# Performance work log

Measured on AMD Instinct MI355X. Metric: run time of the kernel, lower is better.

The kernel has to match this reference:

```python
import jax, jax.numpy as jnp
import numpy as np

N, E, D, H, EF = 50000, 800000, 64, 64, 16


def setup_inputs() -> dict:
    key = jax.random.key(0)
    ks = jax.random.split(key, 12)
    s = 0.05
    return {
        "node_feat": jax.random.normal(ks[0], (N, D), jnp.float32),
        "coord": jax.random.normal(ks[1], (N, 3), jnp.float32),
        "edge_feat": jax.random.normal(ks[2], (E, EF), jnp.float32),
        "src": jax.random.randint(ks[3], (E,), 0, N, jnp.int32),
        "dst": jax.random.randint(ks[4], (E,), 0, N, jnp.int32),
        "W_e1": jax.random.normal(ks[5], (2 * D + EF + 1, H), jnp.float32) * s,
        "b_e1": jnp.zeros((H,), jnp.float32),
        "W_e2": jax.random.normal(ks[6], (H, H), jnp.float32) * s,
        "b_e2": jnp.zeros((H,), jnp.float32),
        "W_n1": jax.random.normal(ks[7], (D + H, H), jnp.float32) * s,
        "b_n1": jnp.zeros((H,), jnp.float32),
        "W_n2": jax.random.normal(ks[8], (H, D), jnp.float32) * s,
        "b_n2": jnp.zeros((D,), jnp.float32),
    }


def reference(node_feat, coord, edge_feat, src, dst,
              W_e1, b_e1, W_e2, b_e2, W_n1, b_n1, W_n2, b_n2):
    # per-edge radial distance: ||coord_src - coord_dst||^2  -> [E,1]
    x_diff = coord[src] - coord[dst]
    radial = jnp.sum(x_diff * x_diff, axis=-1, keepdims=True)
    # edge message MLP: concat [h_src, h_dst, radial, a] -> SiLU MLP
    f = jnp.concatenate([node_feat[src], node_feat[dst], radial, edge_feat], axis=-1)
    m = jax.nn.silu(f @ W_e1 + b_e1)
    msg = jax.nn.silu(m @ W_e2 + b_e2)  # [E,H]
    # scatter-sum aggregation to destination nodes
    h_neigh = jax.ops.segment_sum(msg, dst, num_segments=node_feat.shape[0])
    # node update MLP
    z = jnp.concatenate([node_feat, h_neigh], axis=-1)
    h = jax.nn.silu(z @ W_n1 + b_n1) @ W_n2 + b_n2
    return h
```

## Files before the change

kernel.cpp:

```cpp
#include <hip/hip_runtime.h>

#define D 64
#define H 64
#define EFD 16
#define MS 68
#define TE 128
#define TN 128
#define DPB 16
#define DPB4 32
#define REFW 20

typedef __attribute__((ext_vector_type(8))) short bf16x8;
typedef __attribute__((ext_vector_type(4))) float f32x4;

__device__ __forceinline__ float silu(float x) {
    return x / (1.0f + __expf(-x));
}

__device__ __forceinline__ short f2bf(float x) {
    union { float f; unsigned u; } c; c.f = x;
    unsigned r = c.u + 0x7fffu + ((c.u >> 16) & 1u);
    return (short)(r >> 16);
}

#define GEMM_STEP(acc_, a_, bf_) do { \
    const float* bp_ = (const float*)(bf_); \
    acc_[0] += (a_).x*bp_[0] + (a_).y*bp_[4] + (a_).z*bp_[8]  + (a_).w*bp_[12]; \
    acc_[1] += (a_).x*bp_[1] + (a_).y*bp_[5] + (a_).z*bp_[9]  + (a_).w*bp_[13]; \
    acc_[2] += (a_).x*bp_[2] + (a_).y*bp_[6] + (a_).z*bp_[10] + (a_).w*bp_[14]; \
    acc_[3] += (a_).x*bp_[3] + (a_).y*bp_[7] + (a_).z*bp_[11] + (a_).w*bp_[15]; \
} while (0)

#define PGEMM64(acc_, Wp_, wrow0_, eg_, hg_, smem_) do { \
    for (int k4 = 0; k4 < 16; k4++) { \
        float4 bf_[4]; \
        _Pragma("unroll") \
        for (int kk = 0; kk < 4; kk++) \
            bf_[kk] = *(const float4*)&(Wp_)[(size_t)((wrow0_) + 4*k4 + kk) * H + 4*(hg_)]; \
        _Pragma("unroll") \
        for (int i = 0; i < 8; i++) { \
            float4 a_ = *(const float4*)&(smem_)[(8*(eg_) + i) * MS + 4*k4]; \
            GEMM_STEP(acc_[i], a_, bf_); \
        } \
    } \
} while (0)


__global__ __launch_bounds__(256) void hist_kernel(
    const int* __restrict__ dst, int* __restrict__ deg, int E)
{
    int e = blockIdx.x * 256 + threadIdx.x;
    if (e < E) atomicAdd(&deg[dst[e]], 1);
}


__global__ __launch_bounds__(256) void scanA_kernel(
    const int* __restrict__ deg, int* __restrict__ part, int N)
{
    __shared__ int tmp[256];
    const int tid = threadIdx.x;
    int idx = blockIdx.x * 256 + tid;
    tmp[tid] = (idx < N) ? deg[idx] : 0;
    __syncthreads();
    for (int off = 128; off > 0; off >>= 1) {
        if (tid < off) tmp[tid] += tmp[tid + off];
        __syncthreads();
    }
    if (tid == 0) part[blockIdx.x] = tmp[0];
}

__global__ __launch_bounds__(256, 1) void scanB_kernel(
    int* __restrict__ part, int nparts)
{
    __shared__ int tmp[256];
    __shared__ int carry_s;
    const int tid = threadIdx.x;
    if (tid == 0) carry_s = 0;
    __syncthreads();
    for (int base = 0; base < nparts; base += 256) {
        int idx = base + tid;
        int v = (idx < nparts) ? part[idx] : 0;
        tmp[tid] = v;
        __syncthreads();
        #pragma unroll
        for (int off = 1; off < 256; off <<= 1) {
            int t = (tid >= off) ? tmp[tid - off] : 0;
            __syncthreads();
            tmp[tid] += t;
            __syncthreads();
        }
        int incl = tmp[tid];
        int tot = tmp[255];
        if (idx < nparts) part[idx] = carry_s + incl - v;
        __syncthreads();
        if (tid == 0) carry_s += tot;
        __syncthreads();
    }
}

__global__ __launch_bounds__(256) void scanC_kernel(
    const int* __restrict__ deg, const int* __restrict__ part,
    int* __restrict__ cursor, int N)
{
    __shared__ int tmp[256];
    const int tid = threadIdx.x;
    int idx = blockIdx.x * 256 + tid;
    int v = (idx < N) ? deg[idx] : 0;
    tmp[tid] = v;
    __syncthreads();
    #pragma unroll
    for (int off = 1; off < 256; off <<= 1) {
        int t = (tid >= off) ? tmp[tid - off] : 0;
        __syncthreads();
        tmp[tid] += t;
        __syncthreads();
    }
    if (idx < N) cursor[idx] = part[blockIdx.x] + tmp[tid] - v;
}


__global__ __launch_bounds__(256) void build3_kernel(
    const int* __restrict__ dst, const int* __restrict__ src,
    const float* __restrict__ coord, const float* __restrict__ edge_feat,
    int* __restrict__ cursor,
    int* __restrict__ srcs, int* __restrict__ dsts, float* __restrict__ refr,
    int E)
{
    int e = blockIdx.x * 256 + threadIdx.x;
    if (e >= E) return;
    int d2 = dst[e];
    int s = src[e];
    int pos = atomicAdd(&cursor[d2], 1);
    srcs[pos] = s;
    dsts[pos] = d2;
    float dx = coord[s*3+0] - coord[d2*3+0];
    float dy = coord[s*3+1] - coord[d2*3+1];
    float dz = coord[s*3+2] - coord[d2*3+2];
    float* rr = &refr[(size_t)pos * REFW];
    const float4* ef = (const float4*)&edge_feat[(size_t)e * EFD];
    *(float4*)&rr[0]  = ef[0];
    *(float4*)&rr[4]  = ef[1];
    *(float4*)&rr[8]  = ef[2];
    *(float4*)&rr[12] = ef[3];
    rr[16] = dx*dx + dy*dy + dz*dz;
}

__global__ __launch_bounds__(256) void build2_kernel(
    const int* __restrict__ dst, const int* __restrict__ src,
    int* __restrict__ cursor,
    int* __restrict__ eidx, int* __restrict__ srcs, int* __restrict__ dsts,
    int E)
{
    int e = blockIdx.x * 256 + threadIdx.x;
    if (e < E) {
        int d2 = dst[e];
        int pos = atomicAdd(&cursor[d2], 1);
        eidx[pos] = e;
        srcs[pos] = src[e];
        dsts[pos] = d2;
    }
}


__global__ __launch_bounds__(256, 4) void pre_kernel(
    const float* __restrict__ node_feat,
    const float* __restrict__ W_e1, const float* __restrict__ b_e1,
    float* __restrict__ Pa, float* __restrict__ Pb, int N)
{
    __shared__ float smem[TN * MS];
    const int tid = threadIdx.x;
    const int nbase = blockIdx.x * TN;
    const int ng = tid >> 4, hg = tid & 15, k = tid & 63, no = tid >> 6;

    #pragma unroll
    for (int t = 0; t < 32; t++) {
        int gn = nbase + no + 4*t;
        int cg = (gn < N) ? gn : (N - 1);
        smem[(no + 4*t) * MS + k] = node_feat[(size_t)cg * D + k];
    }
    __syncthreads();

    float accA[8][4], accB[8][4];
    {
        float4 b0 = *(const float4*)&b_e1[4*hg];
        #pragma unroll
        for (int i = 0; i < 8; i++) {
            accA[i][0]=b0.x; accA[i][1]=b0.y; accA[i][2]=b0.z; accA[i][3]=b0.w;
            accB[i][0]=0.f;  accB[i][1]=0.f;  accB[i][2]=0.f;  accB[i][3]=0.f;
        }
    }
    PGEMM64(accA, W_e1, 0,  ng, hg, smem);
    PGEMM64(accB, W_e1, 64, ng, hg, smem);

    #pragma unroll
    for (int i = 0; i < 8; i++) {
        int gn = nbase + 8*ng + i;
        if (gn < N) {
            float4 a; a.x=accA[i][0]; a.y=accA[i][1]; a.z=accA[i][2]; a.w=accA[i][3];
            float4 b; b.x=accB[i][0]; b.y=accB[i][1]; b.z=accB[i][2]; b.w=accB[i][3];
            *(float4*)&Pa[(size_t)gn * H + 4*hg] = a;
            *(float4*)&Pb[(size_t)gn * H + 4*hg] = b;
        }
    }
}


__global__ __launch_bounds__(256, 3) void edge_kernel4(
    const float* __restrict__ Pa, const float* __restrict__ Pb,
    const int* __restrict__ srcs, const int* __restrict__ dsts,
    const float* __restrict__ refr,
    const int* __restrict__ cursor_end, const int* __restrict__ deg,
    const float* __restrict__ W_e1,
    const float* __restrict__ W_e2, const float* __restrict__ b_e2,
    float* __restrict__ h_neigh, int N)
{
    __shared__ alignas(16) short mt[TE * H];
    __shared__ float hacc[DPB4 * H];

    const int tid = threadIdx.x;
    const int lane = tid & 63;
    const int wv = tid >> 6;
    const int lg = lane >> 4;
    const int lc = lane & 15;
    const int eg = tid >> 4;
    const int hg = tid & 15;

    const int dst0 = blockIdx.x * DPB4;
    const int dlast = min(dst0 + DPB4, N) - 1;
    const int rs = cursor_end[dst0] - deg[dst0];
    const int re = cursor_end[dlast];

    for (int i = tid; i < DPB4 * H; i += 256) hacc[i] = 0.f;

    bf16x8 bfr[2][4];
    #pragma unroll
    for (int ks = 0; ks < 2; ks++)
        #pragma unroll
        for (int nf = 0; nf < 4; nf++) {
            bf16x8 v;
            #pragma unroll
            for (int t = 0; t < 8; t++)
                v[t] = f2bf(W_e2[(size_t)(lg*8 + t + 32*ks) * H + 16*nf + lc]);
            bfr[ks][nf] = v;
        }
    float bias[4];
    #pragma unroll
    for (int nf = 0; nf < 4; nf++) bias[nf] = b_e2[16*nf + lc];

    __syncthreads();

    for (int base = rs; base < re; base += TE) {
        float a1[8][4];
        #pragma unroll
        for (int i = 0; i < 8; i++) {
            int p = base + 8*eg + i;
            int pp = (p < re) ? p : (re - 1);
            int s = srcs[pp], d2 = dsts[pp];
            float4 pa = *(const float4*)&Pa[(size_t)s * H + 4*hg];
            float4 pb = *(const float4*)&Pb[(size_t)d2 * H + 4*hg];
            a1[i][0] = pa.x + pb.x; a1[i][1] = pa.y + pb.y;
            a1[i][2] = pa.z + pb.z; a1[i][3] = pa.w + pb.w;
        }
        for (int k4 = 0; k4 < 4; k4++) {
            float4 bf[4];
            #pragma unroll
            for (int kk = 0; kk < 4; kk++)
                bf[kk] = *(const float4*)&W_e1[(size_t)(129 + 4*k4 + kk) * H + 4*hg];
            #pragma unroll
            for (int i = 0; i < 8; i++) {
                int p = base + 8*eg + i;
                int pp = (p < re) ? p : (re - 1);
                float4 a = *(const float4*)&refr[(size_t)pp * REFW + 4*k4];
                GEMM_STEP(a1[i], a, bf);
            }
        }
        {
            float4 b = *(const float4*)&W_e1[(size_t)128 * H + 4*hg];
            #pragma unroll
            for (int i = 0; i < 8; i++) {
                int p = base + 8*eg + i;
                int pp = (p < re) ? p : (re - 1);
                float a = refr[(size_t)pp * REFW + 16];
                a1[i][0] += a*b.x; a1[i][1] += a*b.y;
                a1[i][2] += a*b.z; a1[i][3] += a*b.w;
            }
        }

        #pragma unroll
        for (int i = 0; i < 8; i++) {
            short4 mv;
            mv.x = f2bf(silu(a1[i][0])); mv.y = f2bf(silu(a1[i][1]));
            mv.z = f2bf(silu(a1[i][2])); mv.w = f2bf(silu(a1[i][3]));
            int row = 8*eg + i;
            int sidx = (row * H + 4*hg) ^ (i << 3);
            *(short4*)&mt[sidx] = mv;
        }
        asm volatile("s_waitcnt lgkmcnt(0)" ::: "memory");

        bf16x8 afr[2][2];
        #pragma unroll
        for (int mf = 0; mf < 2; mf++)
            #pragma unroll
            for (int ks = 0; ks < 2; ks++) {
                int row = 32*wv + 16*mf + lc;
                int sidx = (row * H + lg*8 + 32*ks) ^ ((lc & 7) << 3);
                afr[mf][ks] = *(const bf16x8*)&mt[sidx];
            }
        f32x4 c2[2][4];
        #pragma unroll
        for (int mf = 0; mf < 2; mf++)
            #pragma unroll
            for (int nf = 0; nf < 4; nf++) {
                f32x4 cinit = {bias[nf], bias[nf], bias[nf], bias[nf]};
                c2[mf][nf] = cinit;
            }
        #pragma unroll
        for (int ks = 0; ks < 2; ks++)
            #pragma unroll
            for (int mf = 0; mf < 2; mf++)
                #pragma unroll
                for (int nf = 0; nf < 4; nf++)
                    c2[mf][nf] = __builtin_amdgcn_mfma_f32_16x16x32_bf16(
                        afr[mf][ks], bfr[ks][nf], c2[mf][nf], 0, 0, 0);

        #pragma unroll
        for (int mf = 0; mf < 2; mf++) {
            int rb = 32*wv + 16*mf + 4*lg;
            int cur = -1;
            float s0 = 0.f, s1 = 0.f, s2 = 0.f, s3 = 0.f;
            #pragma unroll
            for (int reg = 0; reg < 4; reg++) {
                int p = base + rb + reg;
                if (p < re) {
                    int dl = dsts[p] - dst0;
                    float v0 = silu(c2[mf][0][reg]);
                    float v1 = silu(c2[mf][1][reg]);
                    float v2 = silu(c2[mf][2][reg]);
                    float v3 = silu(c2[mf][3][reg]);
                    if (dl != cur) {
                        if (cur >= 0) {
                            atomicAdd(&hacc[cur*H + lc],      s0);
                            atomicAdd(&hacc[cur*H + 16 + lc], s1);
                            atomicAdd(&hacc[cur*H + 32 + lc], s2);
                            atomicAdd(&hacc[cur*H + 48 + lc], s3);
                        }
                        cur = dl; s0 = v0; s1 = v1; s2 = v2; s3 = v3;
                    } else { s0 += v0; s1 += v1; s2 += v2; s3 += v3; }
                }
            }
            if (cur >= 0) {
                atomicAdd(&hacc[cur*H + lc],      s0);
                atomicAdd(&hacc[cur*H + 16 + lc], s1);
                atomicAdd(&hacc[cur*H + 32 + lc], s2);
                atomicAdd(&hacc[cur*H + 48 + lc], s3);
            }
        }
    }

    __syncthreads();
    #pragma unroll
    for (int t = 0; t < 2; t++) {
        int idx = tid + t*256;
        int dloc = idx >> 4;
        int ch = (idx & 15) * 4;
        int gd = dst0 + dloc;
        if (gd < N)
            *(float4*)&h_neigh[(size_t)gd * H + ch] =
                *(const float4*)&hacc[dloc * H + ch];
    }
}


__global__ __launch_bounds__(256, 4) void edge_kernel2(
    const float* __restrict__ Pa, const float* __restrict__ Pb,
    const float* __restrict__ coord,
    const float* __restrict__ edge_feat,
    const int* __restrict__ eidx, const int* __restrict__ srcs,
    const int* __restrict__ dsts,
    const int* __restrict__ cursor_end, const int* __restrict__ deg,
    const float* __restrict__ W_e1,
    const float* __restrict__ W_e2, const float* __restrict__ b_e2,
    float* __restrict__ h_neigh, int N)
{
    __shared__ float smem[TE * MS];
    __shared__ float hacc[DPB * H];
    __shared__ int ssrc[TE], sdlo[TE], seid[TE];

    const int tid = threadIdx.x;
    const int dst0 = blockIdx.x * DPB;
    const int dlast = min(dst0 + DPB, N) - 1;
    const int rs = cursor_end[dst0] - deg[dst0];
    const int re = cursor_end[dlast];

    for (int i = tid; i < DPB * H; i += 256) hacc[i] = 0.f;

    const int eg = tid >> 4, hg = tid & 15;

    for (int base = rs; base < re; base += TE) {
        const int cnt = min(re - base, TE);
        __syncthreads();

        if (tid < TE) {
            int e = 0, s = 0, dlv = -1;
            float radial = 0.f;
            if (tid < cnt) {
                int p = base + tid;
                e = eidx[p]; s = srcs[p];
                int d2 = dsts[p]; dlv = d2 - dst0;
                float dx = coord[s*3+0] - coord[d2*3+0];
                float dy = coord[s*3+1] - coord[d2*3+1];
                float dz = coord[s*3+2] - coord[d2*3+2];
                radial = dx*dx + dy*dy + dz*dz;
            }
            ssrc[tid] = s; sdlo[tid] = dlv; seid[tid] = e;
            smem[tid * MS + 0] = radial;
        }
        __syncthreads();

        {
            const int k2 = tid & 15, e2 = tid >> 4;
            #pragma unroll
            for (int t = 0; t < 8; t++) {
                int r = e2 + 16*t;
                float v = (sdlo[r] >= 0) ? edge_feat[(size_t)seid[r] * EFD + k2] : 0.f;
                smem[r * MS + 1 + k2] = v;
            }
        }

        float acc[8][4];
        #pragma unroll
        for (int i = 0; i < 8; i++) {
            int r = 8*eg + i;
            int s = ssrc[r];
            int dlv = sdlo[r];
            int drow = (dlv >= 0) ? (dst0 + dlv) : 0;
            float4 pa = *(const float4*)&Pa[(size_t)s * H + 4*hg];
            float4 pb = *(const float4*)&Pb[(size_t)drow * H + 4*hg];
            acc[i][0] = pa.x + pb.x; acc[i][1] = pa.y + pb.y;
            acc[i][2] = pa.z + pb.z; acc[i][3] = pa.w + pb.w;
        }
        __syncthreads();

        for (int k4 = 0; k4 < 4; k4++) {
            float4 bf[4];
            #pragma unroll
            for (int kk = 0; kk < 4; kk++)
                bf[kk] = *(const float4*)&W_e1[(size_t)(128 + 4*k4 + kk) * H + 4*hg];
            #pragma unroll
            for (int i = 0; i < 8; i++) {
                float4 a = *(const float4*)&smem[(8*eg + i) * MS + 4*k4];
                GEMM_STEP(acc[i], a, bf);
            }
        }
        {
            float4 b = *(const float4*)&W_e1[(size_t)144 * H + 4*hg];
            #pragma unroll
            for (int i = 0; i < 8; i++) {
                float a = smem[(8*eg+i)*MS + 16];
                acc[i][0] += a*b.x; acc[i][1] += a*b.y; acc[i][2] += a*b.z; acc[i][3] += a*b.w;
            }
        }
        __syncthreads();

        #pragma unroll
        for (int i = 0; i < 8; i++) {
            float4 mv;
            mv.x = silu(acc[i][0]); mv.y = silu(acc[i][1]);
            mv.z = silu(acc[i][2]); mv.w = silu(acc[i][3]);
            *(float4*)&smem[(8*eg+i)*MS + 4*hg] = mv;
        }
        __syncthreads();

        float acc2[8][4];
        {
            float4 b0 = *(const float4*)&b_e2[4*hg];
            #pragma unroll
            for (int i = 0; i < 8; i++) {
                acc2[i][0]=b0.x; acc2[i][1]=b0.y; acc2[i][2]=b0.z; acc2[i][3]=b0.w;
            }
        }
        PGEMM64(acc2, W_e2, 0, eg, hg, smem);

        float rx=0.f, ry=0.f, rz=0.f, rw=0.f;
        int cur = -1;
        #pragma unroll
        for (int i = 0; i < 8; i++) {
            int r = 8*eg + i;
            int dlv = sdlo[r];
            if (dlv < 0) continue;
            float vx = silu(acc2[i][0]), vy = silu(acc2[i][1]);
            float vz = silu(acc2[i][2]), vw = silu(acc2[i][3]);
            if (dlv != cur) {
                if (cur >= 0) {
                    float* hp = &hacc[cur * H + 4*hg];
                    atomicAdd(&hp[0], rx); atomicAdd(&hp[1], ry);
                    atomicAdd(&hp[2], rz); atomicAdd(&hp[3], rw);
                }
                cur = dlv; rx = vx; ry = vy; rz = vz; rw = vw;
            } else {
                rx += vx; ry += vy; rz += vz; rw += vw;
            }
        }
        if (cur >= 0) {
            float* hp = &hacc[cur * H + 4*hg];
            atomicAdd(&hp[0], rx); atomicAdd(&hp[1], ry);
            atomicAdd(&hp[2], rz); atomicAdd(&hp[3], rw);
        }
    }

    __syncthreads();
    {
        const int dloc = tid >> 4, ch = 4 * (tid & 15);
        int gd = dst0 + dloc;
        if (gd < N) {
            float4 v = *(const float4*)&hacc[dloc * H + ch];
            *(float4*)&h_neigh[(size_t)gd * H + ch] = v;
        }
    }
}


__global__ __launch_bounds__(256, 4) void node_kernel(
    const float* __restrict__ node_feat,
    const float* __restrict__ h_neigh,
    const float* __restrict__ W_n1, const float* __restrict__ b_n1,
    const float* __restrict__ W_n2, const float* __restrict__ b_n2,
    float* __restrict__ out, int N)
{
    __shared__ float smem[TN * MS];

    const int tid = threadIdx.x;
    const int nbase = blockIdx.x * TN;

    const int ng = tid >> 4, hg = tid & 15, k = tid & 63, no = tid >> 6;

    float acc[8][4];
    {
        float4 b0 = *(const float4*)&b_n1[4*hg];
        #pragma unroll
        for (int i = 0; i < 8; i++) {
            acc[i][0]=b0.x; acc[i][1]=b0.y; acc[i][2]=b0.z; acc[i][3]=b0.w;
        }
    }

    float rA[32];
    #pragma unroll
    for (int t = 0; t < 32; t++) {
        int gn = nbase + no + 4*t;
        int cg = (gn < N) ? gn : (N - 1);
        rA[t] = node_feat[(size_t)cg * D + k];
    }
    #pragma unroll
    for (int t = 0; t < 32; t++)
        smem[(no + 4*t) * MS + k] = rA[t];
    __syncthreads();

    float rB[32];
    #pragma unroll
    for (int t = 0; t < 32; t++) {
        int gn = nbase + no + 4*t;
        int cg = (gn < N) ? gn : (N - 1);
        rB[t] = h_neigh[(size_t)cg * H + k];
    }
    PGEMM64(acc, W_n1, 0, ng, hg, smem);
    __syncthreads();

    #pragma unroll
    for (int t = 0; t < 32; t++)
        smem[(no + 4*t) * MS + k] = rB[t];
    __syncthreads();

    PGEMM64(acc, W_n1, 64, ng, hg, smem);
    __syncthreads();

    #pragma unroll
    for (int i = 0; i < 8; i++) {
        float4 mv;
        mv.x = silu(acc[i][0]); mv.y = silu(acc[i][1]);
        mv.z = silu(acc[i][2]); mv.w = silu(acc[i][3]);
        *(float4*)&smem[(8*ng+i)*MS + 4*hg] = mv;
    }
    __syncthreads();

    float acc2[8][4];
    {
        float4 b0 = *(const float4*)&b_n2[4*hg];
        #pragma unroll
        for (int i = 0; i < 8; i++) {
            acc2[i][0]=b0.x; acc2[i][1]=b0.y; acc2[i][2]=b0.z; acc2[i][3]=b0.w;
        }
    }
    PGEMM64(acc2, W_n2, 0, ng, hg, smem);

    #pragma unroll
    for (int i = 0; i < 8; i++) {
        int gn = nbase + 8*ng + i;
        if (gn < N) {
            float4 ov;
            ov.x = acc2[i][0]; ov.y = acc2[i][1]; ov.z = acc2[i][2]; ov.w = acc2[i][3];
            *(float4*)&out[(size_t)gn * D + 4*hg] = ov;
        }
    }
}

extern "C" void kernel_launch(void* const* d_in, const int* in_sizes, int n_in,
                              void* d_out, int out_size, void* d_ws, size_t ws_size,
                              hipStream_t stream)
{
    const float* node_feat = (const float*)d_in[0];
    const float* coord     = (const float*)d_in[1];
    const float* edge_feat = (const float*)d_in[2];
    const int*   src       = (const int*)d_in[3];
    const int*   dst       = (const int*)d_in[4];
    const float* W_e1 = (const float*)d_in[5];
    const float* b_e1 = (const float*)d_in[6];
    const float* W_e2 = (const float*)d_in[7];
    const float* b_e2 = (const float*)d_in[8];
    const float* W_n1 = (const float*)d_in[9];
    const float* b_n1 = (const float*)d_in[10];
    const float* W_n2 = (const float*)d_in[11];
    const float* b_n2 = (const float*)d_in[12];

    const int N = in_sizes[0] / D;
    const int E = in_sizes[3];
    const int NP = (N + 255) / 256;

    const size_t hn_b  = (size_t)N * H * sizeof(float);
    const size_t n_i   = (size_t)N * sizeof(int);
    const size_t e_i   = (size_t)E * sizeof(int);
    const size_t pt_b  = 1024 * sizeof(int);
    const size_t p_b   = (size_t)N * H * sizeof(float);
    const size_t rf_b  = (size_t)E * REFW * sizeof(float);

    const size_t need3 = hn_b + 2*n_i + pt_b + 2*e_i + rf_b + 2*p_b;

    float* h_neigh = (float*)d_ws;

    if (ws_size >= need3) {
        char* p = (char*)d_ws + hn_b;
        int* deg    = (int*)p;   p += n_i;
        int* cursor = (int*)p;   p += n_i;
        int* part   = (int*)p;   p += pt_b;
        int* srcs   = (int*)p;   p += e_i;
        int* dsts   = (int*)p;   p += e_i;
        float* refr = (float*)p; p += rf_b;
        float* Pa   = (float*)p; p += p_b;
        float* Pb   = (float*)p;

        hipMemsetAsync(deg, 0, n_i, stream);
        hist_kernel<<<(E + 255) / 256, 256, 0, stream>>>(dst, deg, E);
        scanA_kernel<<<NP, 256, 0, stream>>>(deg, part, N);
        scanB_kernel<<<1, 256, 0, stream>>>(part, NP);
        scanC_kernel<<<NP, 256, 0, stream>>>(deg, part, cursor, N);
        build3_kernel<<<(E + 255) / 256, 256, 0, stream>>>(dst, src, coord, edge_feat,
                                                           cursor, srcs, dsts, refr, E);
        pre_kernel<<<(N + TN - 1) / TN, 256, 0, stream>>>(node_feat, W_e1, b_e1,
                                                          Pa, Pb, N);
        const int dblocks = (N + DPB4 - 1) / DPB4;
        edge_kernel4<<<dblocks, 256, 0, stream>>>(Pa, Pb, srcs, dsts, refr,
                                                  cursor, deg,
                                                  W_e1, W_e2, b_e2, h_neigh, N);
    } else {
        char* p = (char*)d_ws + hn_b;
        int* deg    = (int*)p;   p += n_i;
        int* cursor = (int*)p;   p += n_i;
        int* part   = (int*)p;   p += pt_b;
        int* eidx   = (int*)p;   p += e_i;
        int* srcs   = (int*)p;   p += e_i;
        int* dsts   = (int*)p;   p += e_i;
        float* Pa   = (float*)p; p += p_b;
        float* Pb   = (float*)p;

        hipMemsetAsync(deg, 0, n_i, stream);
        hist_kernel<<<(E + 255) / 256, 256, 0, stream>>>(dst, deg, E);
        scanA_kernel<<<NP, 256, 0, stream>>>(deg, part, N);
        scanB_kernel<<<1, 256, 0, stream>>>(part, NP);
        scanC_kernel<<<NP, 256, 0, stream>>>(deg, part, cursor, N);
        build2_kernel<<<(E + 255) / 256, 256, 0, stream>>>(dst, src, cursor,
                                                           eidx, srcs, dsts, E);
        pre_kernel<<<(N + TN - 1) / TN, 256, 0, stream>>>(node_feat, W_e1, b_e1,
                                                          Pa, Pb, N);
        const int dblocks2 = (N + DPB - 1) / DPB;
        edge_kernel2<<<dblocks2, 256, 0, stream>>>(Pa, Pb, coord, edge_feat,
                                                   eidx, srcs, dsts, cursor, deg,
                                                   W_e1, W_e2, b_e2, h_neigh, N);
    }

    const int nblocks = (N + TN - 1) / TN;
    node_kernel<<<nblocks, 256, 0, stream>>>(node_feat, h_neigh,
                                             W_n1, b_n1, W_n2, b_n2,
                                             (float*)d_out, N);
}
```

Baseline: 525.8 us.

## Fuse node MLP into edge kernel and drop precomputed edge-record buffer

Removes the build3 pass that wrote a per-edge record (edge features plus radial) in sorted order. The edge kernel now gathers edge_feat through eidx and computes the radial from coord on the fly. The node update MLP is appended to the edge kernel using bf16 MFMA on the block's aggregated h_neigh held in shared memory, which removes the h_neigh global round trip and the separate node_kernel launch. In exchange, edge_feat reads become random gathers, the node MLP runs in bf16, and register pressure in the fused kernel rises.

```diff
diff --git a/kernel.cpp b/kernel.cpp
--- a/kernel.cpp
+++ b/kernel.cpp
@@ -6,9 +6,7 @@
 #define MS 68
 #define TE 128
 #define TN 128
-#define DPB 16
 #define DPB4 32
-#define REFW 20
 
 typedef __attribute__((ext_vector_type(8))) short bf16x8;
 typedef __attribute__((ext_vector_type(4))) float f32x4;
@@ -119,32 +117,6 @@
 }
 
 
-__global__ __launch_bounds__(256) void build3_kernel(
-    const int* __restrict__ dst, const int* __restrict__ src,
-    const float* __restrict__ coord, const float* __restrict__ edge_feat,
-    int* __restrict__ cursor,
-    int* __restrict__ srcs, int* __restrict__ dsts, float* __restrict__ refr,
-    int E)
-{
-    int e = blockIdx.x * 256 + threadIdx.x;
-    if (e >= E) return;
-    int d2 = dst[e];
-    int s = src[e];
-    int pos = atomicAdd(&cursor[d2], 1);
-    srcs[pos] = s;
-    dsts[pos] = d2;
-    float dx = coord[s*3+0] - coord[d2*3+0];
-    float dy = coord[s*3+1] - coord[d2*3+1];
-    float dz = coord[s*3+2] - coord[d2*3+2];
-    float* rr = &refr[(size_t)pos * REFW];
-    const float4* ef = (const float4*)&edge_feat[(size_t)e * EFD];
-    *(float4*)&rr[0]  = ef[0];
-    *(float4*)&rr[4]  = ef[1];
-    *(float4*)&rr[8]  = ef[2];
-    *(float4*)&rr[12] = ef[3];
-    rr[16] = dx*dx + dy*dy + dz*dz;
-}
-
 __global__ __launch_bounds__(256) void build2_kernel(
     const int* __restrict__ dst, const int* __restrict__ src,
     int* __restrict__ cursor,
@@ -205,14 +177,18 @@
 }
 
 
-__global__ __launch_bounds__(256, 3) void edge_kernel4(
+__global__ __launch_bounds__(256, 3) void fused_kernel(
     const float* __restrict__ Pa, const float* __restrict__ Pb,
     const int* __restrict__ srcs, const int* __restrict__ dsts,
-    const float* __restrict__ refr,
+    const int* __restrict__ eidx,
+    const float* __restrict__ edge_feat, const float* __restrict__ coord,
     const int* __restrict__ cursor_end, const int* __restrict__ deg,
     const float* __restrict__ W_e1,
     const float* __restrict__ W_e2, const float* __restrict__ b_e2,
-    float* __restrict__ h_neigh, int N)
+    const float* __restrict__ node_feat,
+    const float* __restrict__ W_n1, const float* __restrict__ b_n1,
+    const float* __restrict__ W_n2, const float* __restrict__ b_n2,
+    float* __restrict__ out, int N)
 {
     __shared__ alignas(16) short mt[TE * H];
     __shared__ float hacc[DPB4 * H];
@@ -250,17 +226,30 @@
     __syncthreads();
 
     for (int base = rs; base < re; base += TE) {
-        float a1[8][4];
+        int sS[8], sD[8], sE[8];
         #pragma unroll
         for (int i = 0; i < 8; i++) {
             int p = base + 8*eg + i;
             int pp = (p < re) ? p : (re - 1);
-            int s = srcs[pp], d2 = dsts[pp];
-            float4 pa = *(const float4*)&Pa[(size_t)s * H + 4*hg];
-            float4 pb = *(const float4*)&Pb[(size_t)d2 * H + 4*hg];
+            sS[i] = srcs[pp]; sD[i] = dsts[pp]; sE[i] = eidx[pp];
+        }
+
+        float a1[8][4];
+        #pragma unroll
+        for (int i = 0; i < 8; i++) {
+            float4 pa = *(const float4*)&Pa[(size_t)sS[i] * H + 4*hg];
+            float4 pb = *(const float4*)&Pb[(size_t)sD[i] * H + 4*hg];
             a1[i][0] = pa.x + pb.x; a1[i][1] = pa.y + pb.y;
             a1[i][2] = pa.z + pb.z; a1[i][3] = pa.w + pb.w;
         }
+        float rad[8];
+        #pragma unroll
+        for (int i = 0; i < 8; i++) {
+            const float* cs = &coord[(size_t)sS[i] * 3];
+            const float* cd = &coord[(size_t)sD[i] * 3];
+            float dx = cs[0]-cd[0], dy = cs[1]-cd[1], dz = cs[2]-cd[2];
+            rad[i] = dx*dx + dy*dy + dz*dz;
+        }
         for (int k4 = 0; k4 < 4; k4++) {
             float4 bf[4];
             #pragma unroll
@@ -268,9 +257,7 @@
                 bf[kk] = *(const float4*)&W_e1[(size_t)(129 + 4*k4 + kk) * H + 4*hg];
             #pragma unroll
             for (int i = 0; i < 8; i++) {
-                int p = base + 8*eg + i;
-                int pp = (p < re) ? p : (re - 1);
-                float4 a = *(const float4*)&refr[(size_t)pp * REFW + 4*k4];
+                float4 a = *(const float4*)&edge_feat[(size_t)sE[i] * EFD + 4*k4];
                 GEMM_STEP(a1[i], a, bf);
             }
         }
@@ -278,11 +265,8 @@
             float4 b = *(const float4*)&W_e1[(size_t)128 * H + 4*hg];
             #pragma unroll
             for (int i = 0; i < 8; i++) {
-                int p = base + 8*eg + i;
-                int pp = (p < re) ? p : (re - 1);
-                float a = refr[(size_t)pp * REFW + 16];
-                a1[i][0] += a*b.x; a1[i][1] += a*b.y;
-                a1[i][2] += a*b.z; a1[i][3] += a*b.w;
+                a1[i][0] += rad[i]*b.x; a1[i][1] += rad[i]*b.y;
+                a1[i][2] += rad[i]*b.z; a1[i][3] += rad[i]*b.w;
             }
         }
 
@@ -311,8 +295,8 @@
         for (int mf = 0; mf < 2; mf++)
             #pragma unroll
             for (int nf = 0; nf < 4; nf++) {
-                f32x4 cinit = {bias[nf], bias[nf], bias[nf], bias[nf]};
-                c2[mf][nf] = cinit;
+                f32x4 ci = {bias[nf], bias[nf], bias[nf], bias[nf]};
+                c2[mf][nf] = ci;
             }
         #pragma unroll
         for (int ks = 0; ks < 2; ks++)
@@ -358,249 +342,101 @@
     }
 
     __syncthreads();
-    #pragma unroll
-    for (int t = 0; t < 2; t++) {
-        int idx = tid + t*256;
-        int dloc = idx >> 4;
-        int ch = (idx & 15) * 4;
-        int gd = dst0 + dloc;
-        if (gd < N)
-            *(float4*)&h_neigh[(size_t)gd * H + ch] =
-                *(const float4*)&hacc[dloc * H + ch];
-    }
-}
-
-
-__global__ __launch_bounds__(256, 4) void edge_kernel2(
-    const float* __restrict__ Pa, const float* __restrict__ Pb,
-    const float* __restrict__ coord,
-    const float* __restrict__ edge_feat,
-    const int* __restrict__ eidx, const int* __restrict__ srcs,
-    const int* __restrict__ dsts,
-    const int* __restrict__ cursor_end, const int* __restrict__ deg,
-    const float* __restrict__ W_e1,
-    const float* __restrict__ W_e2, const float* __restrict__ b_e2,
-    float* __restrict__ h_neigh, int N)
-{
-    __shared__ float smem[TE * MS];
-    __shared__ float hacc[DPB * H];
-    __shared__ int ssrc[TE], sdlo[TE], seid[TE];
-
-    const int tid = threadIdx.x;
-    const int dst0 = blockIdx.x * DPB;
-    const int dlast = min(dst0 + DPB, N) - 1;
-    const int rs = cursor_end[dst0] - deg[dst0];
-    const int re = cursor_end[dlast];
-
-    for (int i = tid; i < DPB * H; i += 256) hacc[i] = 0.f;
-
-    const int eg = tid >> 4, hg = tid & 15;
-
-    for (int base = rs; base < re; base += TE) {
-        const int cnt = min(re - base, TE);
-        __syncthreads();
-
-        if (tid < TE) {
-            int e = 0, s = 0, dlv = -1;
-            float radial = 0.f;
-            if (tid < cnt) {
-                int p = base + tid;
-                e = eidx[p]; s = srcs[p];
-                int d2 = dsts[p]; dlv = d2 - dst0;
-                float dx = coord[s*3+0] - coord[d2*3+0];
-                float dy = coord[s*3+1] - coord[d2*3+1];
-                float dz = coord[s*3+2] - coord[d2*3+2];
-                radial = dx*dx + dy*dy + dz*dz;
-            }
-            ssrc[tid] = s; sdlo[tid] = dlv; seid[tid] = e;
-            smem[tid * MS + 0] = radial;
-        }
-        __syncthreads();
-
-        {
-            const int k2 = tid & 15, e2 = tid >> 4;
-            #pragma unroll
-            for (int t = 0; t < 8; t++) {
-                int r = e2 + 16*t;
-                float v = (sdlo[r] >= 0) ? edge_feat[(size_t)seid[r] * EFD + k2] : 0.f;
-                smem[r * MS + 1 + k2] = v;
-            }
-        }
-
-        float acc[8][4];
-        #pragma unroll
-        for (int i = 0; i < 8; i++) {
-            int r = 8*eg + i;
-            int s = ssrc[r];
-            int dlv = sdlo[r];
-            int drow = (dlv >= 0) ? (dst0 + dlv) : 0;
-            float4 pa = *(const float4*)&Pa[(size_t)s * H + 4*hg];
-            float4 pb = *(const float4*)&Pb[(size_t)drow * H + 4*hg];
-            acc[i][0] = pa.x + pb.x; acc[i][1] = pa.y + pb.y;
-            acc[i][2] = pa.z + pb.z; acc[i][3] = pa.w + pb.w;
-        }
-        __syncthreads();
-
-        for (int k4 = 0; k4 < 4; k4++) {
-            float4 bf[4];
-            #pragma unroll
-            for (int kk = 0; kk < 4; kk++)
-                bf[kk] = *(const float4*)&W_e1[(size_t)(128 + 4*k4 + kk) * H + 4*hg];
-            #pragma unroll
-            for (int i = 0; i < 8; i++) {
-                float4 a = *(const float4*)&smem[(8*eg + i) * MS + 4*k4];
-                GEMM_STEP(acc[i], a, bf);
-            }
-        }
-        {
-            float4 b = *(const float4*)&W_e1[(size_t)144 * H + 4*hg];
-            #pragma unroll
-            for (int i = 0; i < 8; i++) {
-                float a = smem[(8*eg+i)*MS + 16];
-                acc[i][0] += a*b.x; acc[i][1] += a*b.y; acc[i][2] += a*b.z; acc[i][3] += a*b.w;
-            }
-        }
-        __syncthreads();
-
-        #pragma unroll
-        for (int i = 0; i < 8; i++) {
-            float4 mv;
-            mv.x = silu(acc[i][0]); mv.y = silu(acc[i][1]);
-            mv.z = silu(acc[i][2]); mv.w = silu(acc[i][3]);
-            *(float4*)&smem[(8*eg+i)*MS + 4*hg] = mv;
-        }
-        __syncthreads();
-
-        float acc2[8][4];
-        {
-            float4 b0 = *(const float4*)&b_e2[4*hg];
-            #pragma unroll
-            for (int i = 0; i < 8; i++) {
-                acc2[i][0]=b0.x; acc2[i][1]=b0.y; acc2[i][2]=b0.z; acc2[i][3]=b0.w;
-            }
-        }
-        PGEMM64(acc2, W_e2, 0, eg, hg, smem);
-
-        float rx=0.f, ry=0.f, rz=0.f, rw=0.f;
-        int cur = -1;
-        #pragma unroll
-        for (int i = 0; i < 8; i++) {
-            int r = 8*eg + i;
-            int dlv = sdlo[r];
-            if (dlv < 0) continue;
-            float vx = silu(acc2[i][0]), vy = silu(acc2[i][1]);
-            float vz = silu(acc2[i][2]), vw = silu(acc2[i][3]);
-            if (dlv != cur) {
-                if (cur >= 0) {
-                    float* hp = &hacc[cur * H + 4*hg];
-                    atomicAdd(&hp[0], rx); atomicAdd(&hp[1], ry);
-                    atomicAdd(&hp[2], rz); atomicAdd(&hp[3], rw);
-                }
-                cur = dlv; rx = vx; ry = vy; rz = vz; rw = vw;
+
+
+    bf16x8 an[2][4];
+    #pragma unroll
+    for (int mf = 0; mf < 2; mf++) {
+        int row = 16*mf + lc;
+        int gr = dst0 + row; if (gr >= N) gr = N - 1;
+        #pragma unroll
+        for (int ks = 0; ks < 4; ks++) {
+            float4 u0, u1;
+            if (ks < 2) {
+                const float* q = &node_feat[(size_t)gr * D + lg*8 + 32*ks];
+                u0 = *(const float4*)&q[0];
+                u1 = *(const float4*)&q[4];
             } else {
-                rx += vx; ry += vy; rz += vz; rw += vw;
-            }
-        }
-        if (cur >= 0) {
-            float* hp = &hacc[cur * H + 4*hg];
-            atomicAdd(&hp[0], rx); atomicAdd(&hp[1], ry);
-            atomicAdd(&hp[2], rz); atomicAdd(&hp[3], rw);
-        }
-    }
-
-    __syncthreads();
+                const float* q = &hacc[row * H + lg*8 + 32*(ks-2)];
+                u0 = *(const float4*)&q[0];
+                u1 = *(const float4*)&q[4];
+            }
+            bf16x8 v;
+            v[0]=f2bf(u0.x); v[1]=f2bf(u0.y); v[2]=f2bf(u0.z); v[3]=f2bf(u0.w);
+            v[4]=f2bf(u1.x); v[5]=f2bf(u1.y); v[6]=f2bf(u1.z); v[7]=f2bf(u1.w);
+            an[mf][ks] = v;
+        }
+    }
+    bf16x8 bn1[4];
+    #pragma unroll
+    for (int ks = 0; ks < 4; ks++) {
+        bf16x8 v;
+        #pragma unroll
+        for (int t = 0; t < 8; t++)
+            v[t] = f2bf(W_n1[(size_t)(lg*8 + t + 32*ks) * H + 16*wv + lc]);
+        bn1[ks] = v;
+    }
+    float bb1 = b_n1[16*wv + lc];
+    f32x4 c1[2];
     {
-        const int dloc = tid >> 4, ch = 4 * (tid & 15);
-        int gd = dst0 + dloc;
-        if (gd < N) {
-            float4 v = *(const float4*)&hacc[dloc * H + ch];
-            *(float4*)&h_neigh[(size_t)gd * H + ch] = v;
-        }
-    }
-}
-
-
-__global__ __launch_bounds__(256, 4) void node_kernel(
-    const float* __restrict__ node_feat,
-    const float* __restrict__ h_neigh,
-    const float* __restrict__ W_n1, const float* __restrict__ b_n1,
-    const float* __restrict__ W_n2, const float* __restrict__ b_n2,
-    float* __restrict__ out, int N)
-{
-    __shared__ float smem[TN * MS];
-
-    const int tid = threadIdx.x;
-    const int nbase = blockIdx.x * TN;
-
-    const int ng = tid >> 4, hg = tid & 15, k = tid & 63, no = tid >> 6;
-
-    float acc[8][4];
+        f32x4 ci = {bb1, bb1, bb1, bb1};
+        c1[0] = ci; c1[1] = ci;
+    }
+    #pragma unroll
+    for (int ks = 0; ks < 4; ks++)
+        #pragma unroll
+        for (int mf = 0; mf < 2; mf++)
+            c1[mf] = __builtin_amdgcn_mfma_f32_16x16x32_bf16(an[mf][ks], bn1[ks], c1[mf], 0, 0, 0);
+
+    #pragma unroll
+    for (int mf = 0; mf < 2; mf++)
+        #pragma unroll
+        for (int reg = 0; reg < 4; reg++) {
+            int r = 16*mf + 4*lg + reg;
+            int sidx = (r * H + 16*wv + lc) ^ ((r & 7) << 3);
+            mt[sidx] = f2bf(silu(c1[mf][reg]));
+        }
+    __syncthreads();
+
+    bf16x8 a2[2][2];
+    #pragma unroll
+    for (int mf = 0; mf < 2; mf++)
+        #pragma unroll
+        for (int ks = 0; ks < 2; ks++) {
+            int row = 16*mf + lc;
+            int sidx = (row * H + lg*8 + 32*ks) ^ ((lc & 7) << 3);
+            a2[mf][ks] = *(const bf16x8*)&mt[sidx];
+        }
+    bf16x8 bn2[2];
+    #pragma unroll
+    for (int ks = 0; ks < 2; ks++) {
+        bf16x8 v;
+        #pragma unroll
+        for (int t = 0; t < 8; t++)
+            v[t] = f2bf(W_n2[(size_t)(lg*8 + t + 32*ks) * H + 16*wv + lc]);
+        bn2[ks] = v;
+    }
+    float bb2 = b_n2[16*wv + lc];
+    f32x4 co[2];
     {
-        float4 b0 = *(const float4*)&b_n1[4*hg];
-        #pragma unroll
-        for (int i = 0; i < 8; i++) {
-            acc[i][0]=b0.x; acc[i][1]=b0.y; acc[i][2]=b0.z; acc[i][3]=b0.w;
-        }
-    }
-
-    float rA[32];
-    #pragma unroll
-    for (int t = 0; t < 32; t++) {
-        int gn = nbase + no + 4*t;
-        int cg = (gn < N) ? gn : (N - 1);
-        rA[t] = node_feat[(size_t)cg * D + k];
-    }
-    #pragma unroll
-    for (int t = 0; t < 32; t++)
-        smem[(no + 4*t) * MS + k] = rA[t];
-    __syncthreads();
-
-    float rB[32];
-    #pragma unroll
-    for (int t = 0; t < 32; t++) {
-        int gn = nbase + no + 4*t;
-        int cg = (gn < N) ? gn : (N - 1);
-        rB[t] = h_neigh[(size_t)cg * H + k];
-    }
-    PGEMM64(acc, W_n1, 0, ng, hg, smem);
-    __syncthreads();
-
-    #pragma unroll
-    for (int t = 0; t < 32; t++)
-        smem[(no + 4*t) * MS + k] = rB[t];
-    __syncthreads();
-
-    PGEMM64(acc, W_n1, 64, ng, hg, smem);
-    __syncthreads();
-
-    #pragma unroll
-    for (int i = 0; i < 8; i++) {
-        float4 mv;
-        mv.x = silu(acc[i][0]); mv.y = silu(acc[i][1]);
-        mv.z = silu(acc[i][2]); mv.w = silu(acc[i][3]);
-        *(float4*)&smem[(8*ng+i)*MS + 4*hg] = mv;
-    }
-    __syncthreads();
-
-    float acc2[8][4];
-    {
-        float4 b0 = *(const float4*)&b_n2[4*hg];
-        #pragma unroll
-        for (int i = 0; i < 8; i++) {
-            acc2[i][0]=b0.x; acc2[i][1]=b0.y; acc2[i][2]=b0.z; acc2[i][3]=b0.w;
-        }
-    }
-    PGEMM64(acc2, W_n2, 0, ng, hg, smem);
-
-    #pragma unroll
-    for (int i = 0; i < 8; i++) {
-        int gn = nbase + 8*ng + i;
-        if (gn < N) {
-            float4 ov;
-            ov.x = acc2[i][0]; ov.y = acc2[i][1]; ov.z = acc2[i][2]; ov.w = acc2[i][3];
-            *(float4*)&out[(size_t)gn * D + 4*hg] = ov;
-        }
-    }
+        f32x4 ci = {bb2, bb2, bb2, bb2};
+        co[0] = ci; co[1] = ci;
+    }
+    #pragma unroll
+    for (int ks = 0; ks < 2; ks++)
+        #pragma unroll
+        for (int mf = 0; mf < 2; mf++)
+            co[mf] = __builtin_amdgcn_mfma_f32_16x16x32_bf16(a2[mf][ks], bn2[ks], co[mf], 0, 0, 0);
+
+    #pragma unroll
+    for (int mf = 0; mf < 2; mf++)
+        #pragma unroll
+        for (int reg = 0; reg < 4; reg++) {
+            int r = 16*mf + 4*lg + reg;
+            int gn = dst0 + r;
+            if (gn < N)
+                out[(size_t)gn * D + 16*wv + lc] = co[mf][reg];
+        }
 }
 
 extern "C" void kernel_launch(void* const* d_in, const int* in_sizes, int n_in,
@@ -625,69 +461,34 @@
     const int E = in_sizes[3];
     const int NP = (N + 255) / 256;
 
-    const size_t hn_b  = (size_t)N * H * sizeof(float);
-    const size_t n_i   = (size_t)N * sizeof(int);
-    const size_t e_i   = (size_t)E * sizeof(int);
-    const size_t pt_b  = 1024 * sizeof(int);
-    const size_t p_b   = (size_t)N * H * sizeof(float);
-    const size_t rf_b  = (size_t)E * REFW * sizeof(float);
-
-    const size_t need3 = hn_b + 2*n_i + pt_b + 2*e_i + rf_b + 2*p_b;
-
-    float* h_neigh = (float*)d_ws;
-
-    if (ws_size >= need3) {
-        char* p = (char*)d_ws + hn_b;
-        int* deg    = (int*)p;   p += n_i;
-        int* cursor = (int*)p;   p += n_i;
-        int* part   = (int*)p;   p += pt_b;
-        int* srcs   = (int*)p;   p += e_i;
-        int* dsts   = (int*)p;   p += e_i;
-        float* refr = (float*)p; p += rf_b;
-        float* Pa   = (float*)p; p += p_b;
-        float* Pb   = (float*)p;
-
-        hipMemsetAsync(deg, 0, n_i, stream);
-        hist_kernel<<<(E + 255) / 256, 256, 0, stream>>>(dst, deg, E);
-        scanA_kernel<<<NP, 256, 0, stream>>>(deg, part, N);
-        scanB_kernel<<<1, 256, 0, stream>>>(part, NP);
-        scanC_kernel<<<NP, 256, 0, stream>>>(deg, part, cursor, N);
-        build3_kernel<<<(E + 255) / 256, 256, 0, stream>>>(dst, src, coord, edge_feat,
-                                                           cursor, srcs, dsts, refr, E);
-        pre_kernel<<<(N + TN - 1) / TN, 256, 0, stream>>>(node_feat, W_e1, b_e1,
-                                                          Pa, Pb, N);
-        const int dblocks = (N + DPB4 - 1) / DPB4;
-        edge_kernel4<<<dblocks, 256, 0, stream>>>(Pa, Pb, srcs, dsts, refr,
-                                                  cursor, deg,
-                                                  W_e1, W_e2, b_e2, h_neigh, N);
-    } else {
-        char* p = (char*)d_ws + hn_b;
-        int* deg    = (int*)p;   p += n_i;
-        int* cursor = (int*)p;   p += n_i;
-        int* part   = (int*)p;   p += pt_b;
-        int* eidx   = (int*)p;   p += e_i;
-        int* srcs   = (int*)p;   p += e_i;
-        int* dsts   = (int*)p;   p += e_i;
-        float* Pa   = (float*)p; p += p_b;
-        float* Pb   = (float*)p;
-
-        hipMemsetAsync(deg, 0, n_i, stream);
-        hist_kernel<<<(E + 255) / 256, 256, 0, stream>>>(dst, deg, E);
-        scanA_kernel<<<NP, 256, 0, stream>>>(deg, part, N);
-        scanB_kernel<<<1, 256, 0, stream>>>(part, NP);
-        scanC_kernel<<<NP, 256, 0, stream>>>(deg, part, cursor, N);
-        build2_kernel<<<(E + 255) / 256, 256, 0, stream>>>(dst, src, cursor,
-                                                           eidx, srcs, dsts, E);
-        pre_kernel<<<(N + TN - 1) / TN, 256, 0, stream>>>(node_feat, W_e1, b_e1,
-                                                          Pa, Pb, N);
-        const int dblocks2 = (N + DPB - 1) / DPB;
-        edge_kernel2<<<dblocks2, 256, 0, stream>>>(Pa, Pb, coord, edge_feat,
-                                                   eidx, srcs, dsts, cursor, deg,
-                                                   W_e1, W_e2, b_e2, h_neigh, N);
-    }
-
-    const int nblocks = (N + TN - 1) / TN;
-    node_kernel<<<nblocks, 256, 0, stream>>>(node_feat, h_neigh,
-                                             W_n1, b_n1, W_n2, b_n2,
-                                             (float*)d_out, N);
-}
+    const size_t n_i  = (size_t)N * sizeof(int);
+    const size_t e_i  = (size_t)E * sizeof(int);
+    const size_t pt_b = 1024 * sizeof(int);
+    const size_t p_b  = (size_t)N * H * sizeof(float);
+
+    char* p = (char*)d_ws;
+    int* deg    = (int*)p;   p += n_i;
+    int* cursor = (int*)p;   p += n_i;
+    int* part   = (int*)p;   p += pt_b;
+    int* eidx   = (int*)p;   p += e_i;
+    int* srcs   = (int*)p;   p += e_i;
+    int* dsts   = (int*)p;   p += e_i;
+    float* Pa   = (float*)p; p += p_b;
+    float* Pb   = (float*)p;
+
+    hipMemsetAsync(deg, 0, n_i, stream);
+    hist_kernel<<<(E + 255) / 256, 256, 0, stream>>>(dst, deg, E);
+    scanA_kernel<<<NP, 256, 0, stream>>>(deg, part, N);
+    scanB_kernel<<<1, 256, 0, stream>>>(part, NP);
+    scanC_kernel<<<NP, 256, 0, stream>>>(deg, part, cursor, N);
+    build2_kernel<<<(E + 255) / 256, 256, 0, stream>>>(dst, src, cursor,
+                                                       eidx, srcs, dsts, E);
+    pre_kernel<<<(N + TN - 1) / TN, 256, 0, stream>>>(node_feat, W_e1, b_e1,
+                                                      Pa, Pb, N);
+    const int dblocks = (N + DPB4 - 1) / DPB4;
+    fused_kernel<<<dblocks, 256, 0, stream>>>(Pa, Pb, srcs, dsts, eidx,
+                                              edge_feat, coord, cursor, deg,
+                                              W_e1, W_e2, b_e2,
+                                              node_feat, W_n1, b_n1, W_n2, b_n2,
+                                              (float*)d_out, N);
+}
```

Result: no change. 529.7 us (+0.7%).
